# Performance work log

Hardware: AMD Instinct MI355X
Metric: run time of the kernel (lower is better)

## Reference

```python
import jax, jax.numpy as jnp
import numpy as np

B, S, D_IN = 4, 2048, 1024
EMBED, HEADS = 1024, 16
HEAD_DIM = EMBED // HEADS


def setup_inputs() -> dict:
    key = jax.random.key(0)
    k1, k2, k3 = jax.random.split(key, 3)
    x = jax.random.normal(k1, (B, S, D_IN), dtype=jnp.float32)
    # xavier-uniform-ish init scales
    lim_qkv = float(np.sqrt(6.0 / (D_IN + 3 * EMBED)))
    lim_o = float(np.sqrt(6.0 / (EMBED + EMBED)))
    w_qkv = jax.random.uniform(k2, (3 * EMBED, D_IN), minval=-lim_qkv, maxval=lim_qkv, dtype=jnp.float32)
    b_qkv = jnp.zeros((3 * EMBED,), dtype=jnp.float32)
    w_o = jax.random.uniform(k3, (EMBED, EMBED), minval=-lim_o, maxval=lim_o, dtype=jnp.float32)
    b_o = jnp.zeros((EMBED,), dtype=jnp.float32)
    return {"x": x, "w_qkv": w_qkv, "b_qkv": b_qkv, "w_o": w_o, "b_o": b_o}


def reference(x, w_qkv, b_qkv, w_o, b_o):
    b, s, _ = x.shape
    qkv = jnp.einsum('bsi,oi->bso', x, w_qkv) + b_qkv            # (b, s, 3E)
    qkv = qkv.reshape(b, s, HEADS, 3 * HEAD_DIM).transpose(0, 2, 1, 3)  # (b, h, s, 3d)
    q, k, v = jnp.split(qkv, 3, axis=-1)                          # each (b, h, s, d)
    scale = 1.0 / jnp.sqrt(jnp.float32(HEAD_DIM))
    attn = jnp.einsum('bhqd,bhkd->bhqk', q, k) * scale            # (b, h, s, s)
    attn = jax.nn.softmax(attn, axis=-1)
    vals = jnp.einsum('bhqk,bhkd->bhqd', attn, v)                 # (b, h, s, d)
    # NOTE: original torch code reshapes (b,h,s,d) -> (b,s,e) WITHOUT transposing
    # heads back; jnp.reshape reproduces that flattening exactly.
    vals = vals.reshape(b, s, EMBED)
    out = jnp.einsum('bse,oe->bso', vals, w_o) + b_o              # (b, s, E)
    return out
```

## Files before the change

kernel.cpp:

```cpp
#include <hip/hip_runtime.h>
#include <stdint.h>
#include <stddef.h>

#define DEVINL __device__ __forceinline__

typedef unsigned short u16;
typedef unsigned int u32;
typedef __attribute__((ext_vector_type(8))) short short8;
typedef __attribute__((ext_vector_type(4))) float f32x4;
typedef __attribute__((ext_vector_type(4))) u32 u32x4;
typedef __attribute__((ext_vector_type(2))) u32 u32x2;

#define QSCALE 0.18033688011112042f

DEVINL u16 f2bf(float f) {
    u32 u = __builtin_bit_cast(u32, f);
    u32 r = (u + 0x7fffu + ((u >> 16) & 1u)) >> 16;
    return (u16)r;
}

DEVINL void gld_lds16(const void* g, void* l) {
    __builtin_amdgcn_global_load_lds(
        (__attribute__((address_space(1))) u32*)(uintptr_t)g,
        (__attribute__((address_space(3))) u32*)l, 16, 0, 0);
}

DEVINL u32 pack_bf16_trunc(float lo, float hi) {
    return __builtin_amdgcn_perm(__builtin_bit_cast(u32, hi),
                                 __builtin_bit_cast(u32, lo), 0x07060302u);
}

DEVINL void plswap32(u32 &a, u32 &b) {
#if __has_builtin(__builtin_amdgcn_permlane32_swap)
    u32x2 r = __builtin_amdgcn_permlane32_swap(a, b, false, false);
    a = r[0]; b = r[1];
#else
    asm("v_permlane32_swap_b32 %0, %1" : "+v"(a), "+v"(b));
#endif
}
DEVINL void plswap16(u32 &a, u32 &b) {
#if __has_builtin(__builtin_amdgcn_permlane16_swap)
    u32x2 r = __builtin_amdgcn_permlane16_swap(a, b, false, false);
    a = r[0]; b = r[1];
#else
    asm("v_permlane16_swap_b32 %0, %1" : "+v"(a), "+v"(b));
#endif
}

__global__ void prep_inputs(const float* __restrict__ x, const float* __restrict__ wqkv,
                            const float* __restrict__ bqkv, const float* __restrict__ wo,
                            u16* __restrict__ xb, u16* __restrict__ wqb,
                            u16* __restrict__ wob, float* __restrict__ bsc) {
    int blk = blockIdx.x;
    if (blk < 6144) {
        const float* src; u16* dst; int base; bool qscale = false;
        if (blk < 4096)      { src = x;    dst = xb;  base = blk; }
        else if (blk < 5632) { src = wqkv; dst = wqb; base = blk - 4096; qscale = true; }
        else                 { src = wo;   dst = wob; base = blk - 5632; }
        int i = (base * 256 + threadIdx.x) * 8;
        float sc = 1.0f;
        if (qscale) { int row = i >> 10; if ((row % 192) < 64) sc = QSCALE; }
        float4 a = *(const float4*)(src + i);
        float4 c = *(const float4*)(src + i + 4);
        union { u16 s[8]; u32x4 v; } t;
        t.s[0] = f2bf(a.x * sc); t.s[1] = f2bf(a.y * sc); t.s[2] = f2bf(a.z * sc); t.s[3] = f2bf(a.w * sc);
        t.s[4] = f2bf(c.x * sc); t.s[5] = f2bf(c.y * sc); t.s[6] = f2bf(c.z * sc); t.s[7] = f2bf(c.w * sc);
        *(u32x4*)(dst + i) = t.v;
    } else {
        int i = (blk - 6144) * 256 + threadIdx.x;
        float sc = ((i % 192) < 64) ? QSCALE : 1.0f;
        bsc[i] = bqkv[i] * sc;
    }
}

__global__ void gemm_qkv(const u16* __restrict__ A, const u16* __restrict__ Bm,
                         const float* __restrict__ bias, u16* __restrict__ qkvb,
                         u16* __restrict__ vtb) {
    const int K = 1024, N = 3072;
    __shared__ u16 As[128 * 64];
    __shared__ u16 Bs[128 * 64];
    const int tid = threadIdx.x;
    const int lane = tid & 63;
    const int wv = tid >> 6, wr = wv >> 1, wc = wv & 1;
    const int l15 = lane & 15, quad = lane >> 4;
    const int e7 = (l15 & 7) * 8;
    const int id = blockIdx.x;
    const int xcd = id & 7, rr = id >> 3;
    const int m0 = ((xcd << 3) + rr / 24) * 128;
    const int n0 = (rr % 24) * 128;

    f32x4 acc[4][4];
#pragma unroll
    for (int i = 0; i < 4; i++)
#pragma unroll
        for (int j = 0; j < 4; j++) acc[i][j] = (f32x4){0.f, 0.f, 0.f, 0.f};

    const u16* Ab = A + (size_t)m0 * K;
    const u16* Bb = Bm + (size_t)n0 * K;
    const int lrow = lane >> 3;
    const int lgr  = (lane & 7) ^ lrow;
    const int r0   = wv * 8 + lrow;

    for (int k0 = 0; k0 < K; k0 += 64) {
#pragma unroll
        for (int j = 0; j < 4; j++) {
            int row = j * 32 + r0;
            gld_lds16(Ab + (size_t)row * K + k0 + lgr * 8, (char*)As + (size_t)(j * 256 + tid) * 16);
            gld_lds16(Bb + (size_t)row * K + k0 + lgr * 8, (char*)Bs + (size_t)(j * 256 + tid) * 16);
        }
        __syncthreads();
#pragma unroll
        for (int ks = 0; ks < 2; ks++) {
            short8 af[4], bf8[4];
#pragma unroll
            for (int mi = 0; mi < 4; mi++)
                af[mi] = *(const short8*)(As + (wr * 64 + mi * 16 + l15) * 64 + ((ks * 32 + quad * 8) ^ e7));
#pragma unroll
            for (int ni = 0; ni < 4; ni++)
                bf8[ni] = *(const short8*)(Bs + (wc * 64 + ni * 16 + l15) * 64 + ((ks * 32 + quad * 8) ^ e7));
#pragma unroll
            for (int mi = 0; mi < 4; mi++)
#pragma unroll
                for (int ni = 0; ni < 4; ni++)
                    acc[mi][ni] = __builtin_amdgcn_mfma_f32_16x16x32_bf16(af[mi], bf8[ni], acc[mi][ni], 0, 0, 0);
        }
        __syncthreads();
    }

#pragma unroll
    for (int mi = 0; mi < 4; mi++) {
        int row_b = m0 + wr * 64 + mi * 16 + quad * 4;
#pragma unroll
        for (int ni = 0; ni < 4; ni++) {
            int c0 = n0 + wc * 64 + ni * 16;
            int sec0 = c0 % 192;
            float bv = bias[c0 + l15];
            float v0 = acc[mi][ni][0] + bv;
            float v1 = acc[mi][ni][1] + bv;
            float v2 = acc[mi][ni][2] + bv;
            float v3 = acc[mi][ni][3] + bv;
            if (sec0 >= 128) {
                int hh = c0 / 192;
                int b = row_b >> 11;
                int s = row_b & 2047;
                int d = sec0 - 128 + l15;
                u32 lo = (u32)f2bf(v0) | ((u32)f2bf(v1) << 16);
                u32 hi = (u32)f2bf(v2) | ((u32)f2bf(v3) << 16);
                *(u32x2*)(vtb + ((size_t)((b * 16 + hh) * 64 + d)) * 2048 + s) = (u32x2){lo, hi};
            } else {
                int col = c0 + l15;
                qkvb[(size_t)(row_b + 0) * N + col] = f2bf(v0);
                qkvb[(size_t)(row_b + 1) * N + col] = f2bf(v1);
                qkvb[(size_t)(row_b + 2) * N + col] = f2bf(v2);
                qkvb[(size_t)(row_b + 3) * N + col] = f2bf(v3);
            }
        }
    }
}

__global__ void gemm_out(const u16* __restrict__ A, const u16* __restrict__ Bm,
                         const float* __restrict__ bias, float* __restrict__ C) {
    const int K = 1024, N = 1024;
    __shared__ u16 As[128 * 64];
    __shared__ u16 Bs[128 * 64];
    const int tid = threadIdx.x;
    const int lane = tid & 63;
    const int wv = tid >> 6, wr = wv >> 1, wc = wv & 1;
    const int l15 = lane & 15, quad = lane >> 4;
    const int e7 = (l15 & 7) * 8;
    const int id = blockIdx.x;
    const int xcd = id & 7, rr = id >> 3;
    const int m0 = ((xcd << 3) + (rr >> 3)) * 128;
    const int n0 = (rr & 7) * 128;

    f32x4 acc[4][4];
#pragma unroll
    for (int i = 0; i < 4; i++)
#pragma unroll
        for (int j = 0; j < 4; j++) acc[i][j] = (f32x4){0.f, 0.f, 0.f, 0.f};

    const u16* Ab = A + (size_t)m0 * K;
    const u16* Bb = Bm + (size_t)n0 * K;
    const int lrow = lane >> 3;
    const int lgr  = (lane & 7) ^ lrow;
    const int r0   = wv * 8 + lrow;

    for (int k0 = 0; k0 < K; k0 += 64) {
#pragma unroll
        for (int j = 0; j < 4; j++) {
            int row = j * 32 + r0;
            gld_lds16(Ab + (size_t)row * K + k0 + lgr * 8, (char*)As + (size_t)(j * 256 + tid) * 16);
            gld_lds16(Bb + (size_t)row * K + k0 + lgr * 8, (char*)Bs + (size_t)(j * 256 + tid) * 16);
        }
        __syncthreads();
#pragma unroll
        for (int ks = 0; ks < 2; ks++) {
            short8 af[4], bf8[4];
#pragma unroll
            for (int mi = 0; mi < 4; mi++)
                af[mi] = *(const short8*)(As + (wr * 64 + mi * 16 + l15) * 64 + ((ks * 32 + quad * 8) ^ e7));
#pragma unroll
            for (int ni = 0; ni < 4; ni++)
                bf8[ni] = *(const short8*)(Bs + (wc * 64 + ni * 16 + l15) * 64 + ((ks * 32 + quad * 8) ^ e7));
#pragma unroll
            for (int mi = 0; mi < 4; mi++)
#pragma unroll
                for (int ni = 0; ni < 4; ni++)
                    acc[mi][ni] = __builtin_amdgcn_mfma_f32_16x16x32_bf16(af[mi], bf8[ni], acc[mi][ni], 0, 0, 0);
        }
        __syncthreads();
    }

#pragma unroll
    for (int mi = 0; mi < 4; mi++) {
        int row_b = m0 + wr * 64 + mi * 16 + quad * 4;
#pragma unroll
        for (int ni = 0; ni < 4; ni++) {
            int col = n0 + wc * 64 + ni * 16 + l15;
            float bv = bias[col];
#pragma unroll
            for (int r = 0; r < 4; r++)
                C[(size_t)(row_b + r) * N + col] = acc[mi][ni][r] + bv;
        }
    }
}

__launch_bounds__(512, 4)
__global__ void flash_attn(const u16* __restrict__ qkv, const u16* __restrict__ vt,
                           u16* __restrict__ vals2) {
    __shared__ u16 Ks[2][2][64 * 64];
    __shared__ u16 Vts[2][2][64 * 64];

    const int tid = threadIdx.x;
    const int lane = tid & 63, wv = tid >> 6;
    const int l15 = lane & 15, quad = lane >> 4;
    const int e7 = (l15 & 7) * 8;
    const int id = blockIdx.x;
    const int m = id >> 3;
    const int bh = ((id & 7) << 3) + (m >> 3);
    const int s0 = (m & 7) << 8;
    const int b = bh >> 4, h = bh & 15;

    short8 qf[2][2];
    const u16* qbase = qkv + (size_t)(b * 2048 + s0 + wv * 32) * 3072 + h * 192;
#pragma unroll
    for (int qi = 0; qi < 2; qi++)
#pragma unroll
        for (int ks = 0; ks < 2; ks++)
            qf[qi][ks] = *(const short8*)(qbase + (size_t)(qi * 16 + l15) * 3072 + ks * 32 + quad * 8);

    f32x4 o_acc[2][4];
    f32x4 sum_acc[2];
#pragma unroll
    for (int qi = 0; qi < 2; qi++) {
        sum_acc[qi] = (f32x4){0.f, 0.f, 0.f, 0.f};
#pragma unroll
        for (int nd = 0; nd < 4; nd++) o_acc[qi][nd] = (f32x4){0.f, 0.f, 0.f, 0.f};
    }
    const f32x4 fzero = (f32x4){0.f, 0.f, 0.f, 0.f};

    const u16* kg = qkv + (size_t)(b * 2048) * 3072 + h * 192 + 64;
    const u16* vg = vt + (size_t)bh * 64 * 2048;

    const int lrow = lane >> 3;
    const int lgr  = (lane & 7) ^ lrow;
    const int r0   = wv * 8 + lrow;

    const short8 ones = (short8){0x3F80, 0x3F80, 0x3F80, 0x3F80, 0x3F80, 0x3F80, 0x3F80, 0x3F80};

#pragma unroll
    for (int st = 0; st < 2; st++) {
        gld_lds16(kg + (size_t)(st * 64 + r0) * 3072 + lgr * 8,
                  (char*)&Ks[0][st][0] + (size_t)tid * 16);
        gld_lds16(vg + (size_t)r0 * 2048 + st * 64 + lgr * 8,
                  (char*)&Vts[0][st][0] + (size_t)tid * 16);
    }
    __syncthreads();

    int cur = 0;
    for (int kb = 0; kb < 2048; kb += 128) {
        if (kb + 128 < 2048) {
            int nb = cur ^ 1;
#pragma unroll
            for (int st = 0; st < 2; st++) {
                gld_lds16(kg + (size_t)(kb + 128 + st * 64 + r0) * 3072 + lgr * 8,
                          (char*)&Ks[nb][st][0] + (size_t)tid * 16);
                gld_lds16(vg + (size_t)r0 * 2048 + kb + 128 + st * 64 + lgr * 8,
                          (char*)&Vts[nb][st][0] + (size_t)tid * 16);
            }
        }

#pragma unroll
        for (int st = 0; st < 2; st++) {
            const u16* Kc = &Ks[cur][st][0];
            const u16* Vc = &Vts[cur][st][0];

            f32x4 s_acc[4][2];
            __builtin_amdgcn_s_setprio(1);
#pragma unroll
            for (int ki = 0; ki < 4; ki++) {
                short8 kf0 = *(const short8*)(Kc + (ki * 16 + l15) * 64 + ((quad * 8) ^ e7));
                short8 kf1 = *(const short8*)(Kc + (ki * 16 + l15) * 64 + ((32 + quad * 8) ^ e7));
#pragma unroll
                for (int qi = 0; qi < 2; qi++)
                    s_acc[ki][qi] = __builtin_amdgcn_mfma_f32_16x16x32_bf16(kf0, qf[qi][0], fzero, 0, 0, 0);
#pragma unroll
                for (int qi = 0; qi < 2; qi++)
                    s_acc[ki][qi] = __builtin_amdgcn_mfma_f32_16x16x32_bf16(kf1, qf[qi][1], s_acc[ki][qi], 0, 0, 0);
            }
            __builtin_amdgcn_s_setprio(0);

            short8 ap[2][2];
#pragma unroll
            for (int c = 0; c < 2; c++)
#pragma unroll
                for (int qi = 0; qi < 2; qi++) {
                    u32 w0 = pack_bf16_trunc(__builtin_amdgcn_exp2f(s_acc[2 * c][qi][0]),
                                             __builtin_amdgcn_exp2f(s_acc[2 * c][qi][1]));
                    u32 w1 = pack_bf16_trunc(__builtin_amdgcn_exp2f(s_acc[2 * c][qi][2]),
                                             __builtin_amdgcn_exp2f(s_acc[2 * c][qi][3]));
                    u32 w2 = pack_bf16_trunc(__builtin_amdgcn_exp2f(s_acc[2 * c + 1][qi][0]),
                                             __builtin_amdgcn_exp2f(s_acc[2 * c + 1][qi][1]));
                    u32 w3 = pack_bf16_trunc(__builtin_amdgcn_exp2f(s_acc[2 * c + 1][qi][2]),
                                             __builtin_amdgcn_exp2f(s_acc[2 * c + 1][qi][3]));
                    plswap32(w0, w2);
                    plswap32(w1, w3);
                    plswap16(w0, w2);
                    plswap16(w1, w3);
                    u32x4 wf = (u32x4){w0, w1, w2, w3};
                    ap[qi][c] = __builtin_bit_cast(short8, wf);
                }

#pragma unroll
            for (int c = 0; c < 2; c++) {
#pragma unroll
                for (int qi = 0; qi < 2; qi++)
                    sum_acc[qi] = __builtin_amdgcn_mfma_f32_16x16x32_bf16(ap[qi][c], ones, sum_acc[qi], 0, 0, 0);
                __builtin_amdgcn_s_setprio(1);
#pragma unroll
                for (int nd = 0; nd < 4; nd++) {
                    short8 bv = *(const short8*)(Vc + (nd * 16 + l15) * 64 + ((c * 32 + quad * 8) ^ e7));
#pragma unroll
                    for (int qi = 0; qi < 2; qi++)
                        o_acc[qi][nd] = __builtin_amdgcn_mfma_f32_16x16x32_bf16(ap[qi][c], bv, o_acc[qi][nd], 0, 0, 0);
                }
                __builtin_amdgcn_s_setprio(0);
            }
        }

        __syncthreads();
        cur ^= 1;
    }

#pragma unroll
    for (int qi = 0; qi < 2; qi++) {
        f32x4 inv;
#pragma unroll
        for (int r = 0; r < 4; r++) inv[r] = 1.0f / sum_acc[qi][r];
#pragma unroll
        for (int nd = 0; nd < 4; nd++) {
            int d = nd * 16 + l15;
#pragma unroll
            for (int r = 0; r < 4; r++) {
                int s = s0 + wv * 32 + qi * 16 + quad * 4 + r;
                size_t row2 = (size_t)(b * 2048 + h * 128 + (s >> 4));
                int col2 = ((s & 15) << 6) + d;
                vals2[row2 * 1024 + col2] = f2bf(o_acc[qi][nd][r] * inv[r]);
            }
        }
    }
}

extern "C" void kernel_launch(void* const* d_in, const int* in_sizes, int n_in,
                              void* d_out, int out_size, void* d_ws, size_t ws_size,
                              hipStream_t stream) {
    (void)in_sizes; (void)n_in; (void)out_size; (void)ws_size;
    const float* x      = (const float*)d_in[0];
    const float* w_qkv  = (const float*)d_in[1];
    const float* b_qkv  = (const float*)d_in[2];
    const float* w_o    = (const float*)d_in[3];
    const float* b_o    = (const float*)d_in[4];
    float* out = (float*)d_out;

    char* ws = (char*)d_ws;
    u16* xb   = (u16*)(ws);
    u16* wqb  = (u16*)(ws + 16777216);
    u16* wob  = (u16*)(ws + 23068672);
    u16* qkvb = (u16*)(ws + 25165824);
    u16* vtb  = (u16*)(ws + 75497472);
    u16* v2b  = (u16*)(ws + 92274688);
    float* bsc = (float*)(ws + 92274688);

    prep_inputs<<<6156, 256, 0, stream>>>(x, w_qkv, b_qkv, w_o, xb, wqb, wob, bsc);

    gemm_qkv<<<1536, 256, 0, stream>>>(xb, wqb, bsc, qkvb, vtb);

    flash_attn<<<512, 512, 0, stream>>>(qkvb, vtb, v2b);

    gemm_out<<<512, 256, 0, stream>>>(v2b, wob, b_o, out);
}
```

Measured before the change: 244.5 us.

## Double-buffer QKV GEMM LDS tiles and shrink output GEMM N-tile to 64

The QKV projection GEMM now keeps two LDS buffers and prefetches the next K-slab while computing on the current one, with one barrier per iteration. This is meant to hide global-load latency behind MFMA work, at the cost of doubling its LDS footprint and possibly lowering occupancy. Separately, the output GEMM uses 128x64 tiles and 1024 blocks instead of 128x128 and 512, giving more blocks to fill the CUs, at the cost of lower per-block data reuse.

```diff
diff --git a/kernel.cpp b/kernel.cpp
--- a/kernel.cpp
+++ b/kernel.cpp
@@ -77,8 +77,8 @@
                          const float* __restrict__ bias, u16* __restrict__ qkvb,
                          u16* __restrict__ vtb) {
     const int K = 1024, N = 3072;
-    __shared__ u16 As[128 * 64];
-    __shared__ u16 Bs[128 * 64];
+    __shared__ u16 As[2][128 * 64];
+    __shared__ u16 Bs[2][128 * 64];
     const int tid = threadIdx.x;
     const int lane = tid & 63;
     const int wv = tid >> 6, wr = wv >> 1, wc = wv & 1;
@@ -101,23 +101,36 @@
     const int lgr  = (lane & 7) ^ lrow;
     const int r0   = wv * 8 + lrow;
 
+#pragma unroll
+    for (int j = 0; j < 4; j++) {
+        int row = j * 32 + r0;
+        gld_lds16(Ab + (size_t)row * K + lgr * 8, (char*)&As[0][0] + (size_t)(j * 256 + tid) * 16);
+        gld_lds16(Bb + (size_t)row * K + lgr * 8, (char*)&Bs[0][0] + (size_t)(j * 256 + tid) * 16);
+    }
+    __syncthreads();
+
+    int cur = 0;
     for (int k0 = 0; k0 < K; k0 += 64) {
-#pragma unroll
-        for (int j = 0; j < 4; j++) {
-            int row = j * 32 + r0;
-            gld_lds16(Ab + (size_t)row * K + k0 + lgr * 8, (char*)As + (size_t)(j * 256 + tid) * 16);
-            gld_lds16(Bb + (size_t)row * K + k0 + lgr * 8, (char*)Bs + (size_t)(j * 256 + tid) * 16);
-        }
-        __syncthreads();
+        if (k0 + 64 < K) {
+            int nb = cur ^ 1;
+#pragma unroll
+            for (int j = 0; j < 4; j++) {
+                int row = j * 32 + r0;
+                gld_lds16(Ab + (size_t)row * K + k0 + 64 + lgr * 8,
+                          (char*)&As[nb][0] + (size_t)(j * 256 + tid) * 16);
+                gld_lds16(Bb + (size_t)row * K + k0 + 64 + lgr * 8,
+                          (char*)&Bs[nb][0] + (size_t)(j * 256 + tid) * 16);
+            }
+        }
 #pragma unroll
         for (int ks = 0; ks < 2; ks++) {
             short8 af[4], bf8[4];
 #pragma unroll
             for (int mi = 0; mi < 4; mi++)
-                af[mi] = *(const short8*)(As + (wr * 64 + mi * 16 + l15) * 64 + ((ks * 32 + quad * 8) ^ e7));
+                af[mi] = *(const short8*)(&As[cur][0] + (wr * 64 + mi * 16 + l15) * 64 + ((ks * 32 + quad * 8) ^ e7));
 #pragma unroll
             for (int ni = 0; ni < 4; ni++)
-                bf8[ni] = *(const short8*)(Bs + (wc * 64 + ni * 16 + l15) * 64 + ((ks * 32 + quad * 8) ^ e7));
+                bf8[ni] = *(const short8*)(&Bs[cur][0] + (wc * 64 + ni * 16 + l15) * 64 + ((ks * 32 + quad * 8) ^ e7));
 #pragma unroll
             for (int mi = 0; mi < 4; mi++)
 #pragma unroll
@@ -125,6 +138,7 @@
                     acc[mi][ni] = __builtin_amdgcn_mfma_f32_16x16x32_bf16(af[mi], bf8[ni], acc[mi][ni], 0, 0, 0);
         }
         __syncthreads();
+        cur ^= 1;
     }
 
 #pragma unroll
@@ -162,7 +176,7 @@
                          const float* __restrict__ bias, float* __restrict__ C) {
     const int K = 1024, N = 1024;
     __shared__ u16 As[128 * 64];
-    __shared__ u16 Bs[128 * 64];
+    __shared__ u16 Bs[64 * 64];
     const int tid = threadIdx.x;
     const int lane = tid & 63;
     const int wv = tid >> 6, wr = wv >> 1, wc = wv & 1;
@@ -170,14 +184,14 @@
     const int e7 = (l15 & 7) * 8;
     const int id = blockIdx.x;
     const int xcd = id & 7, rr = id >> 3;
-    const int m0 = ((xcd << 3) + (rr >> 3)) * 128;
-    const int n0 = (rr & 7) * 128;
-
-    f32x4 acc[4][4];
+    const int m0 = ((xcd << 3) + (rr >> 4)) * 128;
+    const int n0 = (rr & 15) * 64;
+
+    f32x4 acc[4][2];
 #pragma unroll
     for (int i = 0; i < 4; i++)
 #pragma unroll
-        for (int j = 0; j < 4; j++) acc[i][j] = (f32x4){0.f, 0.f, 0.f, 0.f};
+        for (int j = 0; j < 2; j++) acc[i][j] = (f32x4){0.f, 0.f, 0.f, 0.f};
 
     const u16* Ab = A + (size_t)m0 * K;
     const u16* Bb = Bm + (size_t)n0 * K;
@@ -187,25 +201,27 @@
 
     for (int k0 = 0; k0 < K; k0 += 64) {
 #pragma unroll
-        for (int j = 0; j < 4; j++) {
-            int row = j * 32 + r0;
-            gld_lds16(Ab + (size_t)row * K + k0 + lgr * 8, (char*)As + (size_t)(j * 256 + tid) * 16);
-            gld_lds16(Bb + (size_t)row * K + k0 + lgr * 8, (char*)Bs + (size_t)(j * 256 + tid) * 16);
-        }
+        for (int j = 0; j < 4; j++)
+            gld_lds16(Ab + (size_t)(j * 32 + r0) * K + k0 + lgr * 8,
+                      (char*)As + (size_t)(j * 256 + tid) * 16);
+#pragma unroll
+        for (int j = 0; j < 2; j++)
+            gld_lds16(Bb + (size_t)(j * 32 + r0) * K + k0 + lgr * 8,
+                      (char*)Bs + (size_t)(j * 256 + tid) * 16);
         __syncthreads();
 #pragma unroll
         for (int ks = 0; ks < 2; ks++) {
-            short8 af[4], bf8[4];
+            short8 af[4], bf8[2];
 #pragma unroll
             for (int mi = 0; mi < 4; mi++)
                 af[mi] = *(const short8*)(As + (wr * 64 + mi * 16 + l15) * 64 + ((ks * 32 + quad * 8) ^ e7));
 #pragma unroll
-            for (int ni = 0; ni < 4; ni++)
-                bf8[ni] = *(const short8*)(Bs + (wc * 64 + ni * 16 + l15) * 64 + ((ks * 32 + quad * 8) ^ e7));
+            for (int ni = 0; ni < 2; ni++)
+                bf8[ni] = *(const short8*)(Bs + (wc * 32 + ni * 16 + l15) * 64 + ((ks * 32 + quad * 8) ^ e7));
 #pragma unroll
             for (int mi = 0; mi < 4; mi++)
 #pragma unroll
-                for (int ni = 0; ni < 4; ni++)
+                for (int ni = 0; ni < 2; ni++)
                     acc[mi][ni] = __builtin_amdgcn_mfma_f32_16x16x32_bf16(af[mi], bf8[ni], acc[mi][ni], 0, 0, 0);
         }
         __syncthreads();
@@ -215,8 +231,8 @@
     for (int mi = 0; mi < 4; mi++) {
         int row_b = m0 + wr * 64 + mi * 16 + quad * 4;
 #pragma unroll
-        for (int ni = 0; ni < 4; ni++) {
-            int col = n0 + wc * 64 + ni * 16 + l15;
+        for (int ni = 0; ni < 2; ni++) {
+            int col = n0 + wc * 32 + ni * 16 + l15;
             float bv = bias[col];
 #pragma unroll
             for (int r = 0; r < 4; r++)
@@ -397,5 +413,5 @@
 
     flash_attn<<<512, 512, 0, stream>>>(qkvb, vtb, v2b);
 
-    gemm_out<<<512, 256, 0, stream>>>(v2b, wob, b_o, out);
-}
+    gemm_out<<<1024, 256, 0, stream>>>(v2b, wob, b_o, out);
+}
```

Result: slower. 254.9 us (+4.3%).
